# Kernel tuning notes

Hardware: AMD Instinct MI355X
Metric: run time of the kernel (lower is better)

## Reference

```python
import jax, jax.numpy as jnp
import numpy as np

MAX_SPAN_WIDTH = 30
NUM_WORDS = 2048
NUM_CAND = 8192
HIDDEN = 768
FEAT = 20
FFNN = 1000
SPAN_DIM = HIDDEN * 3 + FEAT  # 2324
TOP_SPAN_NUM = int(NUM_WORDS * 0.4)  # 819


def setup_inputs() -> dict:
    key = jax.random.key(0)
    ks = jax.random.split(key, 16)
    mention_doc = jax.random.normal(ks[0], (NUM_WORDS, HIDDEN), jnp.float32)
    starts = jax.random.randint(ks[1], (NUM_CAND,), 0, NUM_WORDS - MAX_SPAN_WIDTH, jnp.int32)
    widths = jax.random.randint(ks[2], (NUM_CAND,), 1, MAX_SPAN_WIDTH + 1, jnp.int32)
    ends = jnp.minimum(starts + widths - 1, NUM_WORDS - 1).astype(jnp.int32)
    s = 0.02
    lin = lambda k, i, o: jax.random.normal(k, (i, o), jnp.float32) * s
    return dict(
        mention_doc=mention_doc,
        span_width_emb=jax.random.normal(ks[3], (MAX_SPAN_WIDTH, FEAT), jnp.float32) * s,
        head_w=jax.random.normal(ks[4], (HIDDEN,), jnp.float32) * s,
        head_b=jnp.zeros((), jnp.float32),
        m_w1=lin(ks[5], SPAN_DIM, FFNN), m_b1=jnp.zeros((FFNN,), jnp.float32),
        m_w2=lin(ks[6], FFNN, FFNN), m_b2=jnp.zeros((FFNN,), jnp.float32),
        m_w3=jax.random.normal(ks[7], (FFNN,), jnp.float32) * s, m_b3=jnp.zeros((), jnp.float32),
        width_prior_emb=jax.random.normal(ks[8], (MAX_SPAN_WIDTH, FEAT), jnp.float32) * s,
        w_w1=lin(ks[9], FEAT, FFNN), w_b1=jnp.zeros((FFNN,), jnp.float32),
        w_w2=lin(ks[10], FFNN, FFNN), w_b2=jnp.zeros((FFNN,), jnp.float32),
        w_w3=jax.random.normal(ks[11], (FFNN,), jnp.float32) * s, w_b3=jnp.zeros((), jnp.float32),
        candidate_starts=starts,
        candidate_ends=ends,
        top_span_num=TOP_SPAN_NUM,
    )


def get_span_emb(mention_doc, starts, ends, span_width_emb, head_w, head_b):
    # mention_doc: [N, H]; starts/ends: [C]
    num_words = mention_doc.shape[0]
    start_emb = mention_doc[starts]              # [C, H]
    end_emb = mention_doc[ends]                  # [C, H]
    width_ids = ends - starts                    # span width - 1, in [0, MAX_SPAN_WIDTH)
    width_emb = span_width_emb[width_ids]        # [C, F]
    offs = jnp.arange(MAX_SPAN_WIDTH, dtype=starts.dtype)
    idxes = jnp.minimum(starts[:, None] + offs[None, :], num_words - 1)  # [C, W]
    emb_spans = mention_doc[idxes]               # [C, W, H]  (dominant intermediate)
    head_scores = mention_doc @ head_w + head_b  # [N]
    hs = head_scores[idxes]                      # [C, W]
    mask = offs[None, :] <= width_ids[:, None]
    hs = jnp.where(mask, hs, -jnp.inf)
    attn = jax.nn.softmax(hs, axis=1)            # masked softmax over span positions
    attended = jnp.einsum('cw,cwh->ch', attn, emb_spans)
    return jnp.concatenate([start_emb, end_emb, width_emb, attended], axis=-1)  # [C, 3H+F]


def ffnn3(x, w1, b1, w2, b2, w3, b3):
    h = jax.nn.relu(x @ w1 + b1)
    h = jax.nn.relu(h @ w2 + b2)
    return h @ w3 + b3  # [..., ] scalar score per row (Squeezer)


def extract_top_spans(span_scores, starts, ends, top_span_num, num_words):
    # Greedy crossing-interval NMS, faithful to the original sequential algorithm.
    C = span_scores.shape[0]
    order = jnp.argsort(-span_scores)
    offs = jnp.arange(MAX_SPAN_WIDTH, dtype=jnp.int32)

    def body(i, state):
        max_end, min_start, sel, count = state
        idx = order[i]
        s = starts[idx]
        e = ends[idx]
        dup = max_end[s] == e
        j_raw = s + offs
        j = jnp.minimum(j_raw, num_words - 1)
        in_span = j_raw <= e
        # crossing: an already-selected span starting at j>s ends beyond e,
        # or one ending at j<e starts before s.
        c1 = in_span & (j_raw > s) & (max_end[j] > e)
        c2 = in_span & (j_raw < e) & (min_start[j] < s)
        crossed = jnp.any(c1 | c2)
        accept = (~dup) & (~crossed) & (count < top_span_num)
        sel = jnp.where(accept, sel.at[count].set(idx.astype(jnp.int32)), sel)
        max_end = jnp.where(accept, max_end.at[s].max(e), max_end)
        min_start = jnp.where(accept, min_start.at[e].min(s), min_start)
        count = count + accept.astype(jnp.int32)
        return (max_end, min_start, sel, count)

    max_end0 = jnp.full((num_words,), -1, jnp.int32)          # 'not set' sentinel
    min_start0 = jnp.full((num_words,), num_words, jnp.int32)  # 'not set' sentinel
    sel0 = jnp.zeros((top_span_num,), jnp.int32)
    _, _, sel, count = jax.lax.fori_loop(0, C, body, (max_end0, min_start0, sel0, jnp.int32(0)))

    # sort selected spans by (start, end); pad unfilled slots with the first sorted span
    valid = jnp.arange(top_span_num) < count
    keys = jnp.where(valid, starts[sel] * num_words + ends[sel], jnp.iinfo(jnp.int32).max)
    sorted_sel = sel[jnp.argsort(keys)]
    return jnp.where(valid, sorted_sel, sorted_sel[0])


def reference(mention_doc, span_width_emb, head_w, head_b,
              m_w1, m_b1, m_w2, m_b2, m_w3, m_b3,
              width_prior_emb, w_w1, w_b1, w_w2, w_b2, w_w3, w_b3,
              candidate_starts, candidate_ends, top_span_num):
    num_words = mention_doc.shape[0]
    span_emb = get_span_emb(mention_doc, candidate_starts, candidate_ends,
                            span_width_emb, head_w, head_b)            # [C, 2324]
    mention_scores = ffnn3(span_emb, m_w1, m_b1, m_w2, m_b2, m_w3, m_b3)  # [C]
    width_scores = ffnn3(width_prior_emb, w_w1, w_b1, w_w2, w_b2, w_w3, w_b3)  # [30]
    cand_mention_scores = mention_scores + width_scores[candidate_ends - candidate_starts]
    top_idx = extract_top_spans(cand_mention_scores, candidate_starts, candidate_ends,
                                top_span_num, num_words)               # [top]
    top_starts = candidate_starts[top_idx]
    top_ends = candidate_ends[top_idx]
    top_span_emb = span_emb[top_idx]
    top_scores = cand_mention_scores[top_idx]
    return (cand_mention_scores, top_idx, top_starts, top_ends, top_span_emb, top_scores)
```

## Files before the change

### kernel.cpp

```cpp
#include <hip/hip_runtime.h>
#include <cstdio>
#include <cmath>

#define NUM_WORDS 2048
#define NUM_CAND 8192
#define HIDDEN 768
#define FEAT 20
#define FFNN_DIM 1000
#define SPAN_DIM 2324
#define TOP_NUM 819
#define MSW 30
#define KP2 1024
#define NP 1024
#define PNP 3072

#define OUT_TOPIDX   (NUM_CAND)
#define OUT_TSTART   (NUM_CAND + TOP_NUM)
#define OUT_TEND     (NUM_CAND + 2*TOP_NUM)
#define OUT_TEMB     (NUM_CAND + 3*TOP_NUM)
#define OUT_TSCORE   (NUM_CAND + 3*TOP_NUM + TOP_NUM*SPAN_DIM)

typedef short short8 __attribute__((ext_vector_type(8)));
typedef float f32x4 __attribute__((ext_vector_type(4)));
typedef unsigned short u16x4 __attribute__((ext_vector_type(4)));

__device__ __forceinline__ unsigned short bf16_rne(float x) {
    unsigned int u = __float_as_uint(x);
    unsigned int r = u + 0x7FFFu + ((u >> 16) & 1u);
    return (unsigned short)(r >> 16);
}
__device__ __forceinline__ float bf16_to_f(unsigned short h) {
    return __uint_as_float(((unsigned int)h) << 16);
}
__device__ __forceinline__ void store_split2(unsigned short* p0, unsigned short* p1,
                                             size_t off, float v) {
    unsigned short h0 = bf16_rne(v);
    float r1 = v - bf16_to_f(h0);
    p0[off] = h0;
    p1[off] = bf16_rne(r1);
}

__device__ __forceinline__ void gl_lds16(const unsigned short* g, unsigned short* l) {
    __builtin_amdgcn_global_load_lds(
        (const __attribute__((address_space(1))) unsigned short*)g,
        (__attribute__((address_space(3))) unsigned short*)l, 16, 0, 0);
}

__global__ void head_kernel(const float* __restrict__ doc, const float* __restrict__ hw,
                            const float* __restrict__ hb, float* __restrict__ out) {
    int wave = threadIdx.x >> 6, lane = threadIdx.x & 63;
    int row = blockIdx.x * 4 + wave;
    if (row >= NUM_WORDS) return;
    float acc = 0.f;
    for (int h = lane; h < HIDDEN; h += 64) acc += doc[row * HIDDEN + h] * hw[h];
    for (int off = 32; off > 0; off >>= 1) acc += __shfl_down(acc, off);
    if (lane == 0) out[row] = acc + hb[0];
}

__global__ void width_kernel(const float* __restrict__ x, const float* __restrict__ w1,
                             const float* __restrict__ b1, const float* __restrict__ w2,
                             const float* __restrict__ b2, const float* __restrict__ w3,
                             const float* __restrict__ b3, float* __restrict__ out) {
    __shared__ float xs[FEAT];
    __shared__ float h1s[FFNN_DIM];
    __shared__ float red[256];
    int r = blockIdx.x, t = threadIdx.x;
    if (t < FEAT) xs[t] = x[r * FEAT + t];
    __syncthreads();
    for (int j = t; j < FFNN_DIM; j += 256) {
        float acc = b1[j];
        for (int k = 0; k < FEAT; ++k) acc += xs[k] * w1[k * FFNN_DIM + j];
        h1s[j] = fmaxf(acc, 0.f);
    }
    __syncthreads();
    float partial = 0.f;
    for (int j = t; j < FFNN_DIM; j += 256) {
        float acc = b2[j];
        for (int k = 0; k < FFNN_DIM; ++k) acc += h1s[k] * w2[k * FFNN_DIM + j];
        partial += fmaxf(acc, 0.f) * w3[j];
    }
    red[t] = partial;
    __syncthreads();
    for (int s = 128; s > 0; s >>= 1) { if (t < s) red[t] += red[t + s]; __syncthreads(); }
    if (t == 0) out[r] = red[0] + b3[0];
}

__global__ void attn_kernel(const float* __restrict__ head_s, const int* __restrict__ starts,
                            const int* __restrict__ ends, float* __restrict__ attn_g) {
    int wave = threadIdx.x >> 6, w = threadIdx.x & 63;
    int c = blockIdx.x * 4 + wave;
    if (c >= NUM_CAND) return;
    int s = starts[c], e = ends[c];
    int wid = e - s;
    float hsv = -INFINITY;
    if (w < MSW && w <= wid) hsv = head_s[s + w];
    float m = hsv;
    for (int off = 32; off > 0; off >>= 1) m = fmaxf(m, __shfl_down(m, off));
    m = __shfl(m, 0);
    float ex = (w < MSW && w <= wid) ? expf(hsv - m) : 0.f;
    float ssum = ex;
    for (int off = 32; off > 0; off >>= 1) ssum += __shfl_down(ssum, off);
    ssum = __shfl(ssum, 0);
    if (w < 32) attn_g[c * 32 + w] = (w < MSW) ? (ex / ssum) : 0.f;
}

__global__ void doc_convert(const float* __restrict__ doc, unsigned short* __restrict__ d0,
                            unsigned short* __restrict__ d1) {
    int i = blockIdx.x * 256 + threadIdx.x;
    if (i < NUM_WORDS * HIDDEN) store_split2(d0, d1, i, doc[i]);
}

__global__ void convert_wt(const float* __restrict__ w, int K, int N, int Kp,
                           unsigned short* __restrict__ q0, unsigned short* __restrict__ q1) {
    int n = blockIdx.y;
    int k = blockIdx.x * blockDim.x + threadIdx.x;
    if (k >= Kp) return;
    float v = (k < K && n < N) ? w[(size_t)k * N + n] : 0.f;
    store_split2(q0, q1, (size_t)n * Kp + k, v);
}

__global__ void convert_wc(const float* __restrict__ w1,
                           unsigned short* __restrict__ q0, unsigned short* __restrict__ q1) {
    int n2 = blockIdx.y;
    int seg = n2 >> 10;
    int n = n2 & 1023;
    int k = blockIdx.x * 256 + threadIdx.x;
    int row0 = (seg == 0) ? 0 : ((seg == 1) ? HIDDEN : 1556);
    float v = (n < FFNN_DIM) ? w1[(size_t)(row0 + k) * FFNN_DIM + n] : 0.f;
    store_split2(q0, q1, (size_t)n2 * HIDDEN + k, v);
}

__global__ void tw_kernel(const float* __restrict__ swe, const float* __restrict__ w1,
                          float* __restrict__ tw) {
    int wid = blockIdx.x, t = threadIdx.x;
    for (int n = t; n < NP; n += 256) {
        float acc = 0.f;
        if (n < FFNN_DIM) {
            for (int f = 0; f < FEAT; ++f)
                acc += swe[wid * FEAT + f] * w1[(size_t)(1536 + f) * FFNN_DIM + n];
        }
        tw[wid * NP + n] = acc;
    }
}

__device__ __forceinline__ void stage_tile(const unsigned short* __restrict__ src,
                                           unsigned short* lds, int base_row, int Kp, int k0,
                                           int t) {
#pragma unroll
    for (int qi = 0; qi < 2; ++qi) {
        int u = qi * 256 + t;
        int l = u & 63;
        int row = ((u >> 6) << 4) + (l >> 2);
        int cblk = (l & 3) ^ (row & 3);
        const unsigned short* g = src + (size_t)(base_row + row) * Kp + k0 + cblk * 8;
        gl_lds16(g, lds + u * 8);
    }
}

__global__ __launch_bounds__(256, 2) void gemm3p(
    const unsigned short* __restrict__ A0, const unsigned short* __restrict__ A1,
    const unsigned short* __restrict__ B0, const unsigned short* __restrict__ B1,
    float* __restrict__ C) {
    __shared__ unsigned short As0[128 * 32], As1[128 * 32];
    __shared__ unsigned short Bs0[128 * 32], Bs1[128 * 32];
    int t = threadIdx.x;
    int bid = blockIdx.x;
    int bm = (bid & 15) << 7;
    int bn = (bid >> 4) << 7;
    int lane = t & 63, wv = t >> 6;
    int wm = (wv >> 1) * 64, wn = (wv & 1) * 64;
    int lr = lane & 15, qq = lane >> 4;
    int sw = (qq ^ (lr & 3)) * 8;

    f32x4 acc[4][4] = {};

    for (int k0 = 0; k0 < HIDDEN; k0 += 32) {
        stage_tile(A0, As0, bm, HIDDEN, k0, t);
        stage_tile(A1, As1, bm, HIDDEN, k0, t);
        stage_tile(B0, Bs0, bn, HIDDEN, k0, t);
        stage_tile(B1, Bs1, bn, HIDDEN, k0, t);
        __syncthreads();
        short8 a0[4], a1[4];
#pragma unroll
        for (int i = 0; i < 4; ++i) {
            int ra = (wm + i * 16 + lr) * 32 + sw;
            a0[i] = *(const short8*)&As0[ra];
            a1[i] = *(const short8*)&As1[ra];
        }
#pragma unroll
        for (int j = 0; j < 4; ++j) {
            int rb = (wn + j * 16 + lr) * 32 + sw;
            short8 b0 = *(const short8*)&Bs0[rb];
            short8 b1 = *(const short8*)&Bs1[rb];
#pragma unroll
            for (int i = 0; i < 4; ++i) {
                acc[i][j] = __builtin_amdgcn_mfma_f32_16x16x32_bf16(a1[i], b0, acc[i][j], 0, 0, 0);
                acc[i][j] = __builtin_amdgcn_mfma_f32_16x16x32_bf16(a0[i], b1, acc[i][j], 0, 0, 0);
                acc[i][j] = __builtin_amdgcn_mfma_f32_16x16x32_bf16(a0[i], b0, acc[i][j], 0, 0, 0);
            }
        }
        __syncthreads();
    }
#pragma unroll
    for (int i = 0; i < 4; ++i)
#pragma unroll
        for (int j = 0; j < 4; ++j)
#pragma unroll
            for (int r = 0; r < 4; ++r) {
                int m = bm + wm + i * 16 + qq * 4 + r;
                int n = bn + wn + j * 16 + lr;
                C[(size_t)m * PNP + n] = acc[i][j][r];
            }
}

__global__ void combine_kernel(const float* __restrict__ P, const float* __restrict__ tw,
                               const float* __restrict__ attn_g, const float* __restrict__ b1,
                               const int* __restrict__ starts, const int* __restrict__ ends,
                               unsigned short* __restrict__ h0, unsigned short* __restrict__ h1) {
    int c = blockIdx.x, t = threadIdx.x;
    int s = starts[c], e = ends[c];
    int wid = e - s;
    __shared__ float at[MSW];
    if (t < MSW) at[t] = attn_g[c * 32 + t];
    __syncthreads();
    int n0 = t * 4;
    size_t ho = (size_t)c * NP + n0;
    if (t < 250) {
        f32x4 acc = *(const f32x4*)&P[(size_t)s * PNP + n0];
        acc += *(const f32x4*)&P[(size_t)e * PNP + 1024 + n0];
        acc += *(const f32x4*)&tw[(size_t)wid * NP + n0];
        acc += *(const f32x4*)&b1[n0];
        const float* Pa = P + (size_t)s * PNP + 2048 + n0;
        for (int w = 0; w <= wid; ++w)
            acc += at[w] * *(const f32x4*)&Pa[(size_t)w * PNP];
        u16x4 q0, q1;
#pragma unroll
        for (int k = 0; k < 4; ++k) {
            float v = fmaxf(acc[k], 0.f);
            unsigned short x0 = bf16_rne(v);
            float r1 = v - bf16_to_f(x0);
            q0[k] = x0; q1[k] = bf16_rne(r1);
        }
        *(u16x4*)&h0[ho] = q0;
        *(u16x4*)&h1[ho] = q1;
    } else {
        u16x4 z = {0, 0, 0, 0};
        *(u16x4*)&h0[ho] = z;
        *(u16x4*)&h1[ho] = z;
    }
}

__global__ __launch_bounds__(256, 2) void gemm3(
    const unsigned short* __restrict__ A0, const unsigned short* __restrict__ A1,
    const unsigned short* __restrict__ B0, const unsigned short* __restrict__ B1,
    const float* __restrict__ bias, int nreal, int Kp,
    const float* __restrict__ w3, float* __restrict__ partials) {
    __shared__ unsigned short As0[128 * 32], As1[128 * 32];
    __shared__ unsigned short Bs0[128 * 32], Bs1[128 * 32];
    int t = threadIdx.x;
    int bid = blockIdx.x;
    int sm = bid >> 6, idx = bid & 63;
    int bm = ((sm << 3) + (idx & 7)) << 7;
    int bn = (idx >> 3) << 7;
    int lane = t & 63, wv = t >> 6;
    int wm = (wv >> 1) * 64, wn = (wv & 1) * 64;
    int lr = lane & 15, qq = lane >> 4;
    int sw = (qq ^ (lr & 3)) * 8;

    f32x4 acc[4][4] = {};

    for (int k0 = 0; k0 < Kp; k0 += 32) {
        stage_tile(A0, As0, bm, Kp, k0, t);
        stage_tile(A1, As1, bm, Kp, k0, t);
        stage_tile(B0, Bs0, bn, Kp, k0, t);
        stage_tile(B1, Bs1, bn, Kp, k0, t);
        __syncthreads();
        short8 a0[4], a1[4];
#pragma unroll
        for (int i = 0; i < 4; ++i) {
            int ra = (wm + i * 16 + lr) * 32 + sw;
            a0[i] = *(const short8*)&As0[ra];
            a1[i] = *(const short8*)&As1[ra];
        }
#pragma unroll
        for (int j = 0; j < 4; ++j) {
            int rb = (wn + j * 16 + lr) * 32 + sw;
            short8 b0 = *(const short8*)&Bs0[rb];
            short8 b1 = *(const short8*)&Bs1[rb];
#pragma unroll
            for (int i = 0; i < 4; ++i) {
                acc[i][j] = __builtin_amdgcn_mfma_f32_16x16x32_bf16(a1[i], b0, acc[i][j], 0, 0, 0);
                acc[i][j] = __builtin_amdgcn_mfma_f32_16x16x32_bf16(a0[i], b1, acc[i][j], 0, 0, 0);
                acc[i][j] = __builtin_amdgcn_mfma_f32_16x16x32_bf16(a0[i], b0, acc[i][j], 0, 0, 0);
            }
        }
        __syncthreads();
    }

    int pid = ((bn >> 7) << 1) | (wn >> 6);
#pragma unroll
    for (int i = 0; i < 4; ++i)
#pragma unroll
        for (int r = 0; r < 4; ++r) {
            float p = 0.f;
#pragma unroll
            for (int j = 0; j < 4; ++j) {
                int n = bn + wn + j * 16 + lr;
                float v = acc[i][j][r] + (n < nreal ? bias[n] : 0.f);
                v = fmaxf(v, 0.f);
                p += v * (n < nreal ? w3[n] : 0.f);
            }
            p += __shfl_xor(p, 1);
            p += __shfl_xor(p, 2);
            p += __shfl_xor(p, 4);
            p += __shfl_xor(p, 8);
            if (lr == 0) {
                int m = bm + wm + i * 16 + qq * 4 + r;
                partials[(size_t)m * 16 + pid] = p;
            }
        }
}

__global__ void score_final(const float* __restrict__ partials, const float* __restrict__ b3,
                            const float* __restrict__ width_s, const int* __restrict__ starts,
                            const int* __restrict__ ends, float* __restrict__ out) {
    int c = blockIdx.x * 256 + threadIdx.x;
    if (c >= NUM_CAND) return;
    float s = b3[0] + width_s[ends[c] - starts[c]];
#pragma unroll
    for (int p = 0; p < 16; ++p) s += partials[(size_t)c * 16 + p];
    out[c] = s;
}

__global__ __launch_bounds__(256) void rank_kernel(const float* __restrict__ scores,
                                                   const int* __restrict__ starts,
                                                   const int* __restrict__ ends,
                                                   unsigned short* __restrict__ ord_g,
                                                   unsigned int* __restrict__ se_g) {
    __shared__ unsigned long long kk[NUM_CAND];
    int t = threadIdx.x;
    for (int i = t; i < NUM_CAND; i += 256) {
        unsigned int b = __float_as_uint(scores[i]);
        unsigned int u = b ^ ((b & 0x80000000u) ? 0xFFFFFFFFu : 0x80000000u);
        unsigned int hi = ~u;
        kk[i] = ((unsigned long long)hi << 32) | (unsigned int)i;
    }
    __syncthreads();
    int c = blockIdx.x * 32 + (t >> 3);
    int seg = (t & 7) * 1024;
    unsigned long long mykey = kk[c];
    int cnt = 0;
    for (int i = seg; i < seg + 1024; ++i) cnt += (kk[i] < mykey) ? 1 : 0;
    cnt += __shfl_xor(cnt, 1);
    cnt += __shfl_xor(cnt, 2);
    cnt += __shfl_xor(cnt, 4);
    if ((t & 7) == 0) {
        int idx = (int)(mykey & 0xFFFFFFFFull);
        int rank = cnt;
        ord_g[rank] = (unsigned short)idx;
        se_g[rank] = ((unsigned int)starts[idx] << 16) | (unsigned int)ends[idx];
    }
}

__global__ __launch_bounds__(64, 1)
void select_nms(const unsigned int* __restrict__ se_g,
                unsigned short* __restrict__ sel_g,
                int* __restrict__ count_g) {
    __shared__ unsigned int se_arr[NUM_CAND];
    __shared__ unsigned int st[2 * NUM_WORDS];
    int lane = threadIdx.x;

    {
        const uint4* src4 = (const uint4*)se_g;
        uint4* dst4 = (uint4*)se_arr;
        for (int i = lane; i < NUM_CAND / 4; i += 64) dst4[i] = src4[i];
    }
    for (int i = lane; i < 2 * NUM_WORDS; i += 64)
        st[i] = (i & 1) ? (unsigned int)NUM_WORDS : 0u;
    __syncthreads();

    const unsigned long long* stp = (const unsigned long long*)st;
    int count = 0;
    for (int c = 0; c < NUM_CAND / 64; ++c) {
        int ib = c * 64;
        unsigned int sev = se_arr[ib + lane];
        int s = (int)(sev >> 16), e = (int)(sev & 0xFFFFu);
        const unsigned long long* bp = stp + s;
        unsigned long long v[MSW];
#pragma unroll
        for (int w = 0; w < MSW; ++w) v[w] = bp[w];
        int me = (int)(unsigned int)v[0] - 1;
        bool crossedA = (s < e) && ((int)(unsigned int)(v[0] >> 32) < s);
        bool crossedB = false;
#pragma unroll
        for (int w = 1; w < MSW; ++w) {
            int j = s + w;
            bool in = (j <= e);
            int mej = (int)(unsigned int)v[w] - 1;
            int msj = (int)(unsigned int)(v[w] >> 32);
            bool hit = in && ((mej > e) || ((j < e) && (msj < s)));
            if (w & 1) crossedA = crossedA || hit;
            else       crossedB = crossedB || hit;
        }
        bool crossed = crossedA || crossedB;
        bool spec = !crossed && (me != e);

        int cbefore = count;
        unsigned long long window = ~0ull;
        unsigned int pend = 0u;
        int rk = 0, lcnt = 0;
        while (true) {
            unsigned long long b = __ballot(spec) & window;
            if (b == 0ull) break;
            int f = __ffsll((unsigned long long)b) - 1;
            unsigned int sef = __builtin_amdgcn_readlane(sev, (unsigned int)f);
            int sf = (int)(sef >> 16), ef = (int)(sef & 0xFFFFu);
            bool mine = (lane == lcnt);
            pend = mine ? sef : pend;
            rk = mine ? (ib + f) : rk;
            lcnt++;
            count++;
            if (count >= TOP_NUM) break;
            window &= (f >= 63) ? 0ull : (~0ull << (f + 1));
            if (lane > f) {
                if (s == sf) me = max(me, ef);
                crossed = crossed || ((s < sf) && (sf <= e) && (ef > e))
                                  || ((sf < s) && (s <= ef) && (ef < e));
                spec = !crossed && (me != e);
            }
        }
        if (lane < lcnt) {
            int sf = (int)(pend >> 16), ef = (int)(pend & 0xFFFFu);
            sel_g[cbefore + lane] = (unsigned short)rk;
            atomicMax(&st[2 * sf], (unsigned int)(ef + 1));
            atomicMin(&st[2 * ef + 1], (unsigned int)sf);
        }
        if (count >= TOP_NUM) break;
    }
    if (lane == 0) *count_g = count;
}

__global__ __launch_bounds__(256) void select_post(const float* __restrict__ scores,
                                                   const int* __restrict__ starts,
                                                   const int* __restrict__ ends,
                                                   const unsigned short* __restrict__ ord_g,
                                                   const unsigned short* __restrict__ sel_g,
                                                   const int* __restrict__ count_g,
                                                   float* out, int* top_idx_ws) {
    __shared__ unsigned long long fkeys[1024];
    int t = threadIdx.x;
    int count = *count_g;
    for (int i = t; i < 1024; i += 256) {
        unsigned long long k = 0xFFFFFFFFFFFFFFFFull;
        if (i < count) {
            int idx = (int)ord_g[sel_g[i]];
            unsigned int key32 = (unsigned int)(starts[idx] * NUM_WORDS + ends[idx]);
            k = ((unsigned long long)key32 << 32) | (unsigned int)idx;
        }
        fkeys[i] = k;
    }
    __syncthreads();
    for (int size = 2; size <= 1024; size <<= 1) {
        for (int stride = size >> 1; stride > 0; stride >>= 1) {
            for (int i = t; i < 1024; i += 256) {
                int ixj = i ^ stride;
                if (ixj > i) {
                    bool up = ((i & size) == 0);
                    unsigned long long a = fkeys[i], b = fkeys[ixj];
                    if ((a > b) == up) { fkeys[i] = b; fkeys[ixj] = a; }
                }
            }
            __syncthreads();
        }
    }
    for (int i = t; i < TOP_NUM; i += 256) {
        int fi = (i < count) ? (int)(fkeys[i] & 0xFFFFFFFFull)
                             : (int)(fkeys[0] & 0xFFFFFFFFull);
        out[OUT_TOPIDX + i] = (float)fi;
        out[OUT_TSTART + i] = (float)starts[fi];
        out[OUT_TEND + i] = (float)ends[fi];
        out[OUT_TSCORE + i] = scores[fi];
        top_idx_ws[i] = fi;
    }
}

__global__ void gather_emb(const float* __restrict__ doc, const float* __restrict__ swe,
                           const float* __restrict__ attn_g, const int* __restrict__ starts,
                           const int* __restrict__ ends, const int* __restrict__ top_idx_ws,
                           float* __restrict__ out) {
    int r = blockIdx.x, t = threadIdx.x;
    int idx = top_idx_ws[r];
    int s = starts[idx], e = ends[idx];
    int wid = e - s;
    __shared__ float at[MSW];
    if (t < MSW) at[t] = attn_g[(size_t)idx * 32 + t];
    __syncthreads();
    float* dst = out + OUT_TEMB + (size_t)r * SPAN_DIM;
    if (t < 192) {
        int h4 = t * 4;
        f32x4 vs = *(const f32x4*)&doc[(size_t)s * HIDDEN + h4];
        f32x4 ve = *(const f32x4*)&doc[(size_t)e * HIDDEN + h4];
        f32x4 acc = {0.f, 0.f, 0.f, 0.f};
        for (int w = 0; w <= wid; ++w)
            acc += at[w] * *(const f32x4*)&doc[(size_t)(s + w) * HIDDEN + h4];
#pragma unroll
        for (int k = 0; k < 4; ++k) {
            dst[h4 + k] = vs[k];
            dst[HIDDEN + h4 + k] = ve[k];
            dst[2 * HIDDEN + FEAT + h4 + k] = acc[k];
        }
    }
    if (t < FEAT) dst[2 * HIDDEN + t] = swe[wid * FEAT + t];
}

extern "C" void kernel_launch(void* const* d_in, const int* in_sizes, int n_in,
                              void* d_out, int out_size, void* d_ws, size_t ws_size,
                              hipStream_t stream) {
    const float* mention_doc = (const float*)d_in[0];
    const float* span_width_emb = (const float*)d_in[1];
    const float* head_w = (const float*)d_in[2];
    const float* head_b = (const float*)d_in[3];
    const float* m_w1 = (const float*)d_in[4];
    const float* m_b1 = (const float*)d_in[5];
    const float* m_w2 = (const float*)d_in[6];
    const float* m_b2 = (const float*)d_in[7];
    const float* m_w3 = (const float*)d_in[8];
    const float* m_b3 = (const float*)d_in[9];
    const float* width_prior_emb = (const float*)d_in[10];
    const float* w_w1 = (const float*)d_in[11];
    const float* w_b1 = (const float*)d_in[12];
    const float* w_w2 = (const float*)d_in[13];
    const float* w_b2 = (const float*)d_in[14];
    const float* w_w3 = (const float*)d_in[15];
    const float* w_b3 = (const float*)d_in[16];
    const int* cand_starts = (const int*)d_in[17];
    const int* cand_ends = (const int*)d_in[18];

    char* w = (char*)d_ws;
    const size_t szH = (size_t)NUM_CAND * NP * 2;
    const size_t szW2 = (size_t)NP * KP2 * 2;
    const size_t szWc = (size_t)PNP * HIDDEN * 2;
    const size_t szD = (size_t)NUM_WORDS * HIDDEN * 2;
    char* p = w;
    unsigned short* h0 = (unsigned short*)p; p += szH;
    unsigned short* h1 = (unsigned short*)p; p += szH;
    unsigned short* w2t0 = (unsigned short*)p; p += szW2;
    unsigned short* w2t1 = (unsigned short*)p; p += szW2;
    unsigned short* Wc0 = (unsigned short*)p; p += szWc;
    unsigned short* Wc1 = (unsigned short*)p; p += szWc;
    unsigned short* d0 = (unsigned short*)p; p += szD;
    unsigned short* d1 = (unsigned short*)p; p += szD;
    float* P = (float*)p; p += (size_t)NUM_WORDS * PNP * 4;
    float* tw = (float*)p; p += (size_t)MSW * NP * 4;
    float* attn_g = (float*)p; p += (size_t)NUM_CAND * 32 * 4;
    float* partials = (float*)p; p += (size_t)NUM_CAND * 16 * 4;
    unsigned short* ord_g = (unsigned short*)p; p += (size_t)NUM_CAND * 2;
    unsigned int* se_g = (unsigned int*)p; p += (size_t)NUM_CAND * 4;
    unsigned short* sel_g = (unsigned short*)p; p += 2048;
    int* count_g = (int*)p; p += 128;
    float* head_s = (float*)p; p += NUM_WORDS * 4;
    float* width_s = (float*)p; p += 128;
    int* top_idx_ws = (int*)p; p += 4096;

    size_t need = (size_t)(p - w);
    if (ws_size < need) {
        fprintf(stderr, "kernel_launch: ws too small (%zu < %zu)\n", ws_size, need);
    }

    float* out = (float*)d_out;

    head_kernel<<<NUM_WORDS / 4, 256, 0, stream>>>(mention_doc, head_w, head_b, head_s);
    width_kernel<<<MSW, 256, 0, stream>>>(width_prior_emb, w_w1, w_b1, w_w2, w_b2, w_w3, w_b3,
                                          width_s);
    attn_kernel<<<NUM_CAND / 4, 256, 0, stream>>>(head_s, cand_starts, cand_ends, attn_g);
    doc_convert<<<(NUM_WORDS * HIDDEN + 255) / 256, 256, 0, stream>>>(mention_doc, d0, d1);
    convert_wc<<<dim3(3, 3072), 256, 0, stream>>>(m_w1, Wc0, Wc1);
    convert_wt<<<dim3(4, 1024), 256, 0, stream>>>(m_w2, FFNN_DIM, FFNN_DIM, KP2,
                                                  w2t0, w2t1);
    tw_kernel<<<MSW, 256, 0, stream>>>(span_width_emb, m_w1, tw);
    gemm3p<<<16 * 24, 256, 0, stream>>>(d0, d1, Wc0, Wc1, P);
    combine_kernel<<<NUM_CAND, 256, 0, stream>>>(P, tw, attn_g, m_b1, cand_starts, cand_ends,
                                                 h0, h1);
    gemm3<<<512, 256, 0, stream>>>(h0, h1, w2t0, w2t1, m_b2, FFNN_DIM, KP2,
                                   m_w3, partials);
    score_final<<<NUM_CAND / 256, 256, 0, stream>>>(partials, m_b3, width_s, cand_starts,
                                                    cand_ends, out);
    rank_kernel<<<NUM_CAND / 32, 256, 0, stream>>>(out, cand_starts, cand_ends, ord_g, se_g);
    select_nms<<<1, 64, 0, stream>>>(se_g, sel_g, count_g);
    select_post<<<1, 256, 0, stream>>>(out, cand_starts, cand_ends, ord_g, sel_g, count_g,
                                       out, top_idx_ws);
    gather_emb<<<TOP_NUM, 256, 0, stream>>>(mention_doc, span_width_emb, attn_g, cand_starts,
                                            cand_ends, top_idx_ws, out);
}
```

Before: 820.2 us.

## Sort candidates by start for combine locality and tile-transpose weight conversion

Builds a histogram of candidate start positions inside the existing head and attn kernels, then a single-block counting sort produces a permutation of candidates ordered by start. The combine kernel walks candidates through this permutation, with the block index interleaved across 8 groups, so blocks running at the same time read overlapping rows of the projected matrix P and get more cache reuse. The weight conversion kernels are also rewritten to transpose through a padded 64x64 shared-memory tile, giving coalesced reads and writes instead of strided global reads. This adds a serial single-block sort kernel and global atomics to the launch chain.

```diff
diff --git a/kernel.cpp b/kernel.cpp
--- a/kernel.cpp
+++ b/kernel.cpp
@@ -47,7 +47,11 @@
 }
 
 __global__ void head_kernel(const float* __restrict__ doc, const float* __restrict__ hw,
-                            const float* __restrict__ hb, float* __restrict__ out) {
+                            const float* __restrict__ hb, float* __restrict__ out,
+                            int* __restrict__ hist) {
+    if (blockIdx.x == 0) {
+        for (int i = threadIdx.x; i < NUM_WORDS; i += 256) hist[i] = 0;
+    }
     int wave = threadIdx.x >> 6, lane = threadIdx.x & 63;
     int row = blockIdx.x * 4 + wave;
     if (row >= NUM_WORDS) return;
@@ -86,11 +90,13 @@
 }
 
 __global__ void attn_kernel(const float* __restrict__ head_s, const int* __restrict__ starts,
-                            const int* __restrict__ ends, float* __restrict__ attn_g) {
+                            const int* __restrict__ ends, float* __restrict__ attn_g,
+                            int* __restrict__ hist) {
     int wave = threadIdx.x >> 6, w = threadIdx.x & 63;
     int c = blockIdx.x * 4 + wave;
     if (c >= NUM_CAND) return;
     int s = starts[c], e = ends[c];
+    if (w == 0) atomicAdd(&hist[s], 1);
     int wid = e - s;
     float hsv = -INFINITY;
     if (w < MSW && w <= wid) hsv = head_s[s + w];
@@ -104,30 +110,82 @@
     if (w < 32) attn_g[c * 32 + w] = (w < MSW) ? (ex / ssum) : 0.f;
 }
 
+__global__ __launch_bounds__(256) void perm_kernel(const int* __restrict__ hist,
+                                                   const int* __restrict__ starts,
+                                                   int* __restrict__ perm) {
+    __shared__ int hoff[NUM_WORDS];
+    __shared__ int wsum[4];
+    int t = threadIdx.x, lane = t & 63, wv = t >> 6;
+    int base = t * 8;
+    int lh[8];
+    int s0 = 0;
+#pragma unroll
+    for (int i = 0; i < 8; ++i) { lh[i] = hist[base + i]; s0 += lh[i]; }
+    int sc = s0;
+    for (int o = 1; o < 64; o <<= 1) { int v = __shfl_up(sc, o); if (lane >= o) sc += v; }
+    if (lane == 63) wsum[wv] = sc;
+    __syncthreads();
+    int wbase = 0;
+    for (int i = 0; i < wv; ++i) wbase += wsum[i];
+    int run = wbase + sc - s0;
+#pragma unroll
+    for (int i = 0; i < 8; ++i) { hoff[base + i] = run; run += lh[i]; }
+    __syncthreads();
+    for (int c = t; c < NUM_CAND; c += 256) {
+        int pos = atomicAdd(&hoff[starts[c]], 1);
+        perm[pos] = c;
+    }
+}
+
 __global__ void doc_convert(const float* __restrict__ doc, unsigned short* __restrict__ d0,
                             unsigned short* __restrict__ d1) {
     int i = blockIdx.x * 256 + threadIdx.x;
     if (i < NUM_WORDS * HIDDEN) store_split2(d0, d1, i, doc[i]);
 }
 
-__global__ void convert_wt(const float* __restrict__ w, int K, int N, int Kp,
-                           unsigned short* __restrict__ q0, unsigned short* __restrict__ q1) {
-    int n = blockIdx.y;
-    int k = blockIdx.x * blockDim.x + threadIdx.x;
-    if (k >= Kp) return;
-    float v = (k < K && n < N) ? w[(size_t)k * N + n] : 0.f;
-    store_split2(q0, q1, (size_t)n * Kp + k, v);
-}
-
-__global__ void convert_wc(const float* __restrict__ w1,
-                           unsigned short* __restrict__ q0, unsigned short* __restrict__ q1) {
-    int n2 = blockIdx.y;
-    int seg = n2 >> 10;
-    int n = n2 & 1023;
-    int k = blockIdx.x * 256 + threadIdx.x;
+__global__ __launch_bounds__(256) void convert_wc(const float* __restrict__ w1,
+                                                  unsigned short* __restrict__ q0,
+                                                  unsigned short* __restrict__ q1) {
+    __shared__ float tile[64][65];
+    int kbase = blockIdx.x << 6;
+    int n2base = blockIdx.y << 6;
+    int seg = n2base >> 10;
+    int nbase = n2base & 1023;
     int row0 = (seg == 0) ? 0 : ((seg == 1) ? HIDDEN : 1556);
-    float v = (n < FFNN_DIM) ? w1[(size_t)(row0 + k) * FFNN_DIM + n] : 0.f;
-    store_split2(q0, q1, (size_t)n2 * HIDDEN + k, v);
+    int t = threadIdx.x;
+    int c = t & 63, r0 = t >> 6;
+    for (int rr = 0; rr < 64; rr += 4) {
+        int r = rr + r0;
+        int n = nbase + c;
+        tile[r][c] = (n < FFNN_DIM) ? w1[(size_t)(row0 + kbase + r) * FFNN_DIM + n] : 0.f;
+    }
+    __syncthreads();
+    int kl = t & 63;
+    for (int rr = 0; rr < 64; rr += 4) {
+        int nl = rr + r0;
+        store_split2(q0, q1, (size_t)(n2base + nl) * HIDDEN + kbase + kl, tile[kl][nl]);
+    }
+}
+
+__global__ __launch_bounds__(256) void convert_wt(const float* __restrict__ w,
+                                                  unsigned short* __restrict__ q0,
+                                                  unsigned short* __restrict__ q1) {
+    __shared__ float tile[64][65];
+    int kbase = blockIdx.x << 6;
+    int nbase = blockIdx.y << 6;
+    int t = threadIdx.x;
+    int c = t & 63, r0 = t >> 6;
+    for (int rr = 0; rr < 64; rr += 4) {
+        int r = rr + r0;
+        int k = kbase + r, n = nbase + c;
+        tile[r][c] = (k < FFNN_DIM && n < FFNN_DIM) ? w[(size_t)k * FFNN_DIM + n] : 0.f;
+    }
+    __syncthreads();
+    int kl = t & 63;
+    for (int rr = 0; rr < 64; rr += 4) {
+        int nl = rr + r0;
+        store_split2(q0, q1, (size_t)(nbase + nl) * KP2 + kbase + kl, tile[kl][nl]);
+    }
 }
 
 __global__ void tw_kernel(const float* __restrict__ swe, const float* __restrict__ w1,
@@ -216,8 +274,11 @@
 __global__ void combine_kernel(const float* __restrict__ P, const float* __restrict__ tw,
                                const float* __restrict__ attn_g, const float* __restrict__ b1,
                                const int* __restrict__ starts, const int* __restrict__ ends,
+                               const int* __restrict__ perm,
                                unsigned short* __restrict__ h0, unsigned short* __restrict__ h1) {
-    int c = blockIdx.x, t = threadIdx.x;
+    int pos = ((blockIdx.x & 7) << 10) | (blockIdx.x >> 3);
+    int c = perm[pos];
+    int t = threadIdx.x;
     int s = starts[c], e = ends[c];
     int wid = e - s;
     __shared__ float at[MSW];
@@ -561,6 +622,8 @@
     float* head_s = (float*)p; p += NUM_WORDS * 4;
     float* width_s = (float*)p; p += 128;
     int* top_idx_ws = (int*)p; p += 4096;
+    int* hist_g = (int*)p; p += NUM_WORDS * 4;
+    int* perm_g = (int*)p; p += (size_t)NUM_CAND * 4;
 
     size_t need = (size_t)(p - w);
     if (ws_size < need) {
@@ -569,18 +632,20 @@
 
     float* out = (float*)d_out;
 
-    head_kernel<<<NUM_WORDS / 4, 256, 0, stream>>>(mention_doc, head_w, head_b, head_s);
+    head_kernel<<<NUM_WORDS / 4, 256, 0, stream>>>(mention_doc, head_w, head_b, head_s,
+                                                   hist_g);
     width_kernel<<<MSW, 256, 0, stream>>>(width_prior_emb, w_w1, w_b1, w_w2, w_b2, w_w3, w_b3,
                                           width_s);
-    attn_kernel<<<NUM_CAND / 4, 256, 0, stream>>>(head_s, cand_starts, cand_ends, attn_g);
+    attn_kernel<<<NUM_CAND / 4, 256, 0, stream>>>(head_s, cand_starts, cand_ends, attn_g,
+                                                  hist_g);
     doc_convert<<<(NUM_WORDS * HIDDEN + 255) / 256, 256, 0, stream>>>(mention_doc, d0, d1);
-    convert_wc<<<dim3(3, 3072), 256, 0, stream>>>(m_w1, Wc0, Wc1);
-    convert_wt<<<dim3(4, 1024), 256, 0, stream>>>(m_w2, FFNN_DIM, FFNN_DIM, KP2,
-                                                  w2t0, w2t1);
+    convert_wc<<<dim3(12, 48), 256, 0, stream>>>(m_w1, Wc0, Wc1);
+    convert_wt<<<dim3(16, 16), 256, 0, stream>>>(m_w2, w2t0, w2t1);
     tw_kernel<<<MSW, 256, 0, stream>>>(span_width_emb, m_w1, tw);
+    perm_kernel<<<1, 256, 0, stream>>>(hist_g, cand_starts, perm_g);
     gemm3p<<<16 * 24, 256, 0, stream>>>(d0, d1, Wc0, Wc1, P);
     combine_kernel<<<NUM_CAND, 256, 0, stream>>>(P, tw, attn_g, m_b1, cand_starts, cand_ends,
-                                                 h0, h1);
+                                                 perm_g, h0, h1);
     gemm3<<<512, 256, 0, stream>>>(h0, h1, w2t0, w2t1, m_b2, FFNN_DIM, KP2,
                                    m_w3, partials);
     score_final<<<NUM_CAND / 256, 256, 0, stream>>>(partials, m_b3, width_s, cand_starts,
```

Result: faster. 792.9 us (-3.3%).
